# Optimization experiments

Hardware: AMD Instinct MI355X
Metric: run time of the kernel (lower is better)

Reference implementation:

```python
import jax, jax.numpy as jnp
import numpy as np

M1, N1, M2, N2, RANK = 64, 64, 64, 64, 256
TOKENS = 8192  # batch 4 * seq 2048, flattened


def setup_inputs() -> dict:
    key = jax.random.key(0)
    k_x, k_c1, k_c2, k_b = jax.random.split(key, 4)
    x = jax.random.normal(k_x, (TOKENS, N1 * N2), dtype=jnp.float32)
    # scale cores so reconstructed weight has reasonable magnitude
    core1 = jax.random.normal(k_c1, (M1, N1, RANK), dtype=jnp.float32) * 0.05
    core2 = jax.random.normal(k_c2, (RANK, M2, N2), dtype=jnp.float32) * 0.05
    bias = jax.random.normal(k_b, (M1 * M2,), dtype=jnp.float32)
    return {"x": x, "core1": core1, "core2": core2, "bias": bias}


def reference(x, core1, core2, bias):
    # contract_mpo: [m1,n1,r] x [r,m2,n2] -> [m1,n1,m2,n2]
    t = jnp.einsum('mnr,rpq->mnpq', core1, core2)
    # permute(0,2,1,3) then view -> weight [m1*m2, n1*n2] = [out, in]
    weight = t.transpose(0, 2, 1, 3).reshape(M1 * M2, N1 * N2)
    # nn.functional.linear: x @ W^T + b
    return x @ weight.T + bias
```

## Files before the change

### kernel.cpp

```cpp
#include <hip/hip_runtime.h>
#include <hip/hip_bf16.h>
#include <stdint.h>


#define TOKENS 8192
#define DIN    4096
#define DOUT   4096
#define RANK   256
#define GEMM_K 4096

typedef __attribute__((ext_vector_type(8))) short   short8;
typedef __attribute__((ext_vector_type(4))) float   floatx4;

__device__ __forceinline__ unsigned short f2bf(float f) {
  union { float f; unsigned u; } v; v.f = f;
  unsigned r = v.u + 0x7FFFu + ((v.u >> 16) & 1u);
  return (unsigned short)(r >> 16);
}

__device__ __forceinline__ void gl2lds16(const void* g, void* l) {
  __builtin_amdgcn_global_load_lds(
      (const __attribute__((address_space(1))) unsigned int*)g,
      (__attribute__((address_space(3))) unsigned int*)l,
      16, 0, 0);
}

__global__ __launch_bounds__(256) void k_f32_to_bf16(const float* __restrict__ src,
                                                     unsigned short* __restrict__ dst,
                                                     int n) {
  int i = (blockIdx.x * 256 + threadIdx.x) * 8;
  if (i >= n) return;
  float4 a = *(const float4*)(src + i);
  float4 b = *(const float4*)(src + i + 4);
  short8 o;
  o[0] = (short)f2bf(a.x); o[1] = (short)f2bf(a.y);
  o[2] = (short)f2bf(a.z); o[3] = (short)f2bf(a.w);
  o[4] = (short)f2bf(b.x); o[5] = (short)f2bf(b.y);
  o[6] = (short)f2bf(b.z); o[7] = (short)f2bf(b.w);
  *(short8*)(dst + i) = o;
}

__global__ __launch_bounds__(256) void k_transpose_c2(const float* __restrict__ c2,
                                                      unsigned short* __restrict__ c2t) {
  __shared__ float tile[64][65];
  const int p0 = blockIdx.x * 64;
  const int r0 = blockIdx.y * 64;
  {
    const int px = threadIdx.x & 63;
    const int rb = threadIdx.x >> 6;
    for (int s = 0; s < 16; ++s) {
      int r = rb + s * 4;
      tile[r][px] = c2[(size_t)(r0 + r) * 4096 + p0 + px];
    }
  }
  __syncthreads();
  {
    const int rx = threadIdx.x & 63;
    const int pb = threadIdx.x >> 6;
    for (int s = 0; s < 16; ++s) {
      int p = pb + s * 4;
      c2t[(size_t)(p0 + p) * 256 + r0 + rx] = f2bf(tile[rx][p]);
    }
  }
}

template <int K, int BK, bool PERM>
__global__ __launch_bounds__(256) void k_gemm_bt(const unsigned short* __restrict__ A,
                                                 const unsigned short* __restrict__ B,
                                                 float* __restrict__ outF,
                                                 unsigned short* __restrict__ outW,
                                                 const float* __restrict__ bias) {
  constexpr int ROWB   = BK * 2;
  constexpr int CM     = BK / 8 - 1;
  constexpr int ROUNDS = BK / 16;
  constexpr int KK     = BK / 32;

  __shared__ __align__(16) unsigned short As[128 * BK];
  __shared__ __align__(16) unsigned short Bs[128 * BK];

  const int tid  = threadIdx.x;
  const int lane = tid & 63;
  const int wave = tid >> 6;
  const int m0 = blockIdx.y * 128;
  const int n0 = blockIdx.x * 128;

  const int waveM = (wave & 1) * 64;
  const int waveN = (wave >> 1) * 64;
  const int l15  = lane & 15;
  const int quad = lane >> 4;

  floatx4 acc[4][4];
#pragma unroll
  for (int i = 0; i < 4; ++i)
#pragma unroll
    for (int j = 0; j < 4; ++j) acc[i][j] = (floatx4)0.0f;

  const size_t rowBytes = (size_t)K * 2;

  for (int kt = 0; kt < K; kt += BK) {
    __syncthreads();
#pragma unroll
    for (int j = 0; j < ROUNDS; ++j) {
      const int flat = (j * 4 + wave) * 1024 + lane * 16;
      const int row  = flat / ROWB;
      const int c    = (flat >> 4) & CM;
      const int cs   = c ^ (row & CM);
      const int ldsb = (j * 4 + wave) * 1024;
      gl2lds16((const char*)A + (size_t)(m0 + row) * rowBytes + (size_t)kt * 2 + cs * 16,
               (char*)As + ldsb);
      gl2lds16((const char*)B + (size_t)(n0 + row) * rowBytes + (size_t)kt * 2 + cs * 16,
               (char*)Bs + ldsb);
    }
    __syncthreads();

#pragma unroll
    for (int kk = 0; kk < KK; ++kk) {
      short8 af[4], bfr[4];
#pragma unroll
      for (int mi = 0; mi < 4; ++mi) {
        const int row = waveM + mi * 16 + l15;
        const int cs  = (kk * 4 + quad) ^ (row & CM);
        af[mi] = *(const short8*)(As + row * BK + cs * 8);
      }
#pragma unroll
      for (int ni = 0; ni < 4; ++ni) {
        const int row = waveN + ni * 16 + l15;
        const int cs  = (kk * 4 + quad) ^ (row & CM);
        bfr[ni] = *(const short8*)(Bs + row * BK + cs * 8);
      }
#pragma unroll
      for (int mi = 0; mi < 4; ++mi)
#pragma unroll
        for (int ni = 0; ni < 4; ++ni)
          acc[mi][ni] = __builtin_amdgcn_mfma_f32_16x16x32_bf16(af[mi], bfr[ni], acc[mi][ni], 0, 0, 0);
    }
  }

  if (!PERM) {
#pragma unroll
    for (int ni = 0; ni < 4; ++ni) {
      const int col = n0 + waveN + ni * 16 + l15;
      const float bv = bias[col];
#pragma unroll
      for (int mi = 0; mi < 4; ++mi) {
        const int rowb = m0 + waveM + mi * 16 + quad * 4;
#pragma unroll
        for (int r = 0; r < 4; ++r)
          outF[(size_t)(rowb + r) * DOUT + col] = acc[mi][ni][r] + bv;
      }
    }
  } else {
#pragma unroll
    for (int ni = 0; ni < 4; ++ni) {
      const int bcol = n0 + waveN + ni * 16 + l15;
      const int m2 = bcol >> 6, n2 = bcol & 63;
#pragma unroll
      for (int mi = 0; mi < 4; ++mi) {
        const int arow0 = m0 + waveM + mi * 16 + quad * 4;
#pragma unroll
        for (int r = 0; r < 4; ++r) {
          const int arow = arow0 + r;
          const int m1 = arow >> 6, n1 = arow & 63;
          outW[(size_t)(m1 * 64 + m2) * 4096 + (n1 * 64 + n2)] = f2bf(acc[mi][ni][r]);
        }
      }
    }
  }
}


__global__ __launch_bounds__(512, 2) void k_gemm256(const unsigned short* __restrict__ A,
                                                    const unsigned short* __restrict__ B,
                                                    float* __restrict__ out,
                                                    const float* __restrict__ bias) {
  __shared__ __align__(16) unsigned short As[2][2][8192];
  __shared__ __align__(16) unsigned short Bs[2][2][8192];

  const int tid  = threadIdx.x;
  const int lane = tid & 63;
  const int wave = tid >> 6;

  const int id  = blockIdx.y * gridDim.x + blockIdx.x;
  const int nid = (id & 7) * 64 + (id >> 3);
  const int bx  = nid & 15;
  const int by  = nid >> 4;
  const int m0  = by * 256;
  const int n0  = bx * 256;

  const int waveM = (wave >> 2) << 7;
  const int waveN = (wave & 3) << 6;
  const int l15   = lane & 15;
  const int quad  = lane >> 4;

  const int rsw = (quad ^ ((l15 >> 2) & 2)) * 8;
  const int srow   = wave * 16 + (lane >> 2);
  const int schunk = (lane & 3) ^ ((lane >> 4) & 2);

  floatx4 acc[8][4];
#pragma unroll
  for (int i = 0; i < 8; ++i)
#pragma unroll
    for (int j = 0; j < 4; ++j) acc[i][j] = (floatx4)0.0f;

#define STAGE(LDSHALF, GBASE, R0, KBYTE)                                          \
  {                                                                               \
    _Pragma("unroll")                                                             \
    for (int j_ = 0; j_ < 2; ++j_) {                                              \
      const char* src_ = (const char*)(GBASE) +                                   \
          (size_t)((R0) + j_ * 128 + srow) * (size_t)(GEMM_K * 2) +               \
          (size_t)(KBYTE) + schunk * 16;                                          \
      gl2lds16(src_, (char*)(LDSHALF) + j_ * 8192 + wave * 1024);                 \
    }                                                                             \
  }

#define PHASE(BUF, KH, MH, DO_STAGE, DO_VMCNT)                                    \
  {                                                                               \
    const unsigned short* pa_ = &As[BUF][KH][0];                                  \
    short8 af_[4];                                                                \
    if ((MH) == 0) {                                                              \
      const unsigned short* pb_ = &Bs[BUF][KH][0];                                \
      _Pragma("unroll")                                                           \
      for (int i_ = 0; i_ < 4; ++i_)                                              \
        bfv[i_] = *(const short8*)(pb_ + (waveN + i_ * 16 + l15) * 32 + rsw);     \
    }                                                                             \
    _Pragma("unroll")                                                             \
    for (int i_ = 0; i_ < 4; ++i_)                                                \
      af_[i_] = *(const short8*)(pa_ + (waveM + ((MH) * 4 + i_) * 16 + l15) * 32 + rsw); \
    DO_STAGE;                                                                     \
    if (DO_VMCNT) asm volatile("s_waitcnt vmcnt(4)" ::: "memory");                \
    asm volatile("s_barrier" ::: "memory");                                       \
    __builtin_amdgcn_sched_barrier(0);                                            \
    __builtin_amdgcn_s_setprio(1);                                                \
    _Pragma("unroll")                                                             \
    for (int i_ = 0; i_ < 4; ++i_)                                                \
      _Pragma("unroll")                                                           \
      for (int n_ = 0; n_ < 4; ++n_)                                              \
        acc[(MH) * 4 + i_][n_] = __builtin_amdgcn_mfma_f32_16x16x32_bf16(         \
            af_[i_], bfv[n_], acc[(MH) * 4 + i_][n_], 0, 0, 0);                   \
    __builtin_amdgcn_s_setprio(0);                                                \
    asm volatile("s_barrier" ::: "memory");                                       \
  }

#define KTILE(C, KTN)                                                             \
  {                                                                               \
    PHASE(C, 0, 0, STAGE(&As[1 - (C)][0][0], A, m0, (KTN) * 2), 0)                \
    PHASE(C, 0, 1, STAGE(&Bs[1 - (C)][0][0], B, n0, (KTN) * 2), 1)                \
    PHASE(C, 1, 0, STAGE(&As[1 - (C)][1][0], A, m0, (KTN) * 2 + 64), 0)           \
    PHASE(C, 1, 1, STAGE(&Bs[1 - (C)][1][0], B, n0, (KTN) * 2 + 64), 1)           \
  }

  STAGE(&As[0][0][0], A, m0, 0);
  STAGE(&Bs[0][0][0], B, n0, 0);
  STAGE(&As[0][1][0], A, m0, 64);
  STAGE(&Bs[0][1][0], B, n0, 64);
  asm volatile("s_waitcnt vmcnt(0)" ::: "memory");
  asm volatile("s_barrier" ::: "memory");

  short8 bfv[4];
  for (int kt = 0; kt < GEMM_K; kt += 128) {
    const int ktn0 = kt + 64;
    KTILE(0, ktn0)
    const int ktn1 = (kt + 128 < GEMM_K) ? (kt + 128) : 0;
    KTILE(1, ktn1)
  }

#undef KTILE
#undef PHASE
#undef STAGE

#pragma unroll
  for (int ni = 0; ni < 4; ++ni) {
    const int col = n0 + waveN + ni * 16 + l15;
    const float bv = bias[col];
#pragma unroll
    for (int mi = 0; mi < 8; ++mi) {
      const int row0 = m0 + waveM + mi * 16 + quad * 4;
#pragma unroll
      for (int r = 0; r < 4; ++r)
        out[(size_t)(row0 + r) * DOUT + col] = acc[mi][ni][r] + bv;
    }
  }
}

extern "C" void kernel_launch(void* const* d_in, const int* in_sizes, int n_in,
                              void* d_out, int out_size, void* d_ws, size_t ws_size,
                              hipStream_t stream) {
  const float* x    = (const float*)d_in[0];
  const float* c1   = (const float*)d_in[1];
  const float* c2   = (const float*)d_in[2];
  const float* bias = (const float*)d_in[3];
  float* out = (float*)d_out;

  char* ws = (char*)d_ws;
  unsigned short* xb  = (unsigned short*)ws;
  unsigned short* Wb  = (unsigned short*)(ws + 67108864);
  unsigned short* c1b = (unsigned short*)(ws + 67108864 + 33554432);
  unsigned short* c2t = (unsigned short*)(ws + 67108864 + 33554432 + 2097152);

  k_f32_to_bf16<<<(TOKENS * DIN) / 2048, 256, 0, stream>>>(x, xb, TOKENS * DIN);
  k_f32_to_bf16<<<(64 * 64 * RANK) / 2048, 256, 0, stream>>>(c1, c1b, 64 * 64 * RANK);
  k_transpose_c2<<<dim3(64, 4), 256, 0, stream>>>(c2, c2t);

  k_gemm_bt<RANK, 32, true><<<dim3(32, 32), 256, 0, stream>>>(c1b, c2t, nullptr, Wb, nullptr);
  k_gemm256<<<dim3(16, 32), 512, 0, stream>>>(xb, Wb, out, bias);
}
```

Before: 509.9 us.

## Software-pipeline LDS fragment reads with MFMA and cut barriers per k-tile

Restructures the GEMM main loop so the A/B fragments for the next MFMA group are read from LDS while the current group computes. Double-buffered register fragments (af0/af1, bfvA/bfvB) are added, and the number of barriers per k-tile drops from eight to two, with a vmcnt(2) wait. This targets LDS-read latency and barrier stalls. In exchange it uses more registers, which could pressure occupancy at 2 blocks of 512 threads per CU, and the sync placement must keep the reads of the next buffer correctly ordered.

```diff
diff --git a/kernel.cpp b/kernel.cpp
--- a/kernel.cpp
+++ b/kernel.cpp
@@ -168,7 +168,6 @@
   }
 }
 
-
 __global__ __launch_bounds__(512, 2) void k_gemm256(const unsigned short* __restrict__ A,
                                                     const unsigned short* __restrict__ B,
                                                     float* __restrict__ out,
@@ -201,6 +200,8 @@
   for (int i = 0; i < 8; ++i)
 #pragma unroll
     for (int j = 0; j < 4; ++j) acc[i][j] = (floatx4)0.0f;
+
+  short8 af0[4], af1[4], bfvA[4], bfvB[4];
 
 #define STAGE(LDSHALF, GBASE, R0, KBYTE)                                          \
   {                                                                               \
@@ -213,40 +214,57 @@
     }                                                                             \
   }
 
-#define PHASE(BUF, KH, MH, DO_STAGE, DO_VMCNT)                                    \
-  {                                                                               \
-    const unsigned short* pa_ = &As[BUF][KH][0];                                  \
-    short8 af_[4];                                                                \
-    if ((MH) == 0) {                                                              \
-      const unsigned short* pb_ = &Bs[BUF][KH][0];                                \
-      _Pragma("unroll")                                                           \
-      for (int i_ = 0; i_ < 4; ++i_)                                              \
-        bfv[i_] = *(const short8*)(pb_ + (waveN + i_ * 16 + l15) * 32 + rsw);     \
-    }                                                                             \
+#define READ_AF(DST, BUF, KH, MH)                                                 \
+  _Pragma("unroll")                                                               \
+  for (int i_ = 0; i_ < 4; ++i_)                                                  \
+    DST[i_] = *(const short8*)(&As[BUF][KH][0] +                                  \
+               (waveM + ((MH) * 4 + i_) * 16 + l15) * 32 + rsw);
+
+#define READ_BF(DST, BUF, KH)                                                     \
+  _Pragma("unroll")                                                               \
+  for (int n_ = 0; n_ < 4; ++n_)                                                  \
+    DST[n_] = *(const short8*)(&Bs[BUF][KH][0] +                                  \
+               (waveN + n_ * 16 + l15) * 32 + rsw);
+
+#define MFMA16(AF, BF, MH)                                                        \
+  __builtin_amdgcn_s_setprio(1);                                                  \
+  _Pragma("unroll")                                                               \
+  for (int i_ = 0; i_ < 4; ++i_)                                                  \
     _Pragma("unroll")                                                             \
-    for (int i_ = 0; i_ < 4; ++i_)                                                \
-      af_[i_] = *(const short8*)(pa_ + (waveM + ((MH) * 4 + i_) * 16 + l15) * 32 + rsw); \
-    DO_STAGE;                                                                     \
-    if (DO_VMCNT) asm volatile("s_waitcnt vmcnt(4)" ::: "memory");                \
-    asm volatile("s_barrier" ::: "memory");                                       \
+    for (int n_ = 0; n_ < 4; ++n_)                                                \
+      acc[(MH) * 4 + i_][n_] = __builtin_amdgcn_mfma_f32_16x16x32_bf16(           \
+          AF[i_], BF[n_], acc[(MH) * 4 + i_][n_], 0, 0, 0);                       \
+  __builtin_amdgcn_s_setprio(0);
+
+#define SYNC2()                                                                   \
+  asm volatile("s_waitcnt vmcnt(2)" ::: "memory");                                \
+  asm volatile("s_barrier" ::: "memory");
+
+#define KTILE(C, KTN)                                                             \
+  {                        \
+    READ_AF(af1, C, 0, 1)                                                         \
+    STAGE(&As[1 - (C)][0][0], A, m0, (KTN) * 2)                                   \
     __builtin_amdgcn_sched_barrier(0);                                            \
-    __builtin_amdgcn_s_setprio(1);                                                \
-    _Pragma("unroll")                                                             \
-    for (int i_ = 0; i_ < 4; ++i_)                                                \
-      _Pragma("unroll")                                                           \
-      for (int n_ = 0; n_ < 4; ++n_)                                              \
-        acc[(MH) * 4 + i_][n_] = __builtin_amdgcn_mfma_f32_16x16x32_bf16(         \
-            af_[i_], bfv[n_], acc[(MH) * 4 + i_][n_], 0, 0, 0);                   \
-    __builtin_amdgcn_s_setprio(0);                                                \
-    asm volatile("s_barrier" ::: "memory");                                       \
-  }
-
-#define KTILE(C, KTN)                                                             \
-  {                                                                               \
-    PHASE(C, 0, 0, STAGE(&As[1 - (C)][0][0], A, m0, (KTN) * 2), 0)                \
-    PHASE(C, 0, 1, STAGE(&Bs[1 - (C)][0][0], B, n0, (KTN) * 2), 1)                \
-    PHASE(C, 1, 0, STAGE(&As[1 - (C)][1][0], A, m0, (KTN) * 2 + 64), 0)           \
-    PHASE(C, 1, 1, STAGE(&Bs[1 - (C)][1][0], B, n0, (KTN) * 2 + 64), 1)           \
+    MFMA16(af0, bfvA, 0)                                                          \
+                \
+    SYNC2()                                                                       \
+    READ_AF(af0, C, 1, 0)                                                         \
+    READ_BF(bfvB, C, 1)                                                           \
+    STAGE(&Bs[1 - (C)][0][0], B, n0, (KTN) * 2)                                   \
+    __builtin_amdgcn_sched_barrier(0);                                            \
+    MFMA16(af1, bfvA, 1)                                                          \
+                           \
+    READ_AF(af1, C, 1, 1)                                                         \
+    STAGE(&As[1 - (C)][1][0], A, m0, (KTN) * 2 + 64)                              \
+    __builtin_amdgcn_sched_barrier(0);                                            \
+    MFMA16(af0, bfvB, 0)                                                          \
+    \
+    SYNC2()                                                                       \
+    READ_AF(af0, 1 - (C), 0, 0)                                                   \
+    READ_BF(bfvA, 1 - (C), 0)                                                     \
+    STAGE(&Bs[1 - (C)][1][0], B, n0, (KTN) * 2 + 64)                              \
+    __builtin_amdgcn_sched_barrier(0);                                            \
+    MFMA16(af1, bfvB, 1)                                                          \
   }
 
   STAGE(&As[0][0][0], A, m0, 0);
@@ -255,17 +273,20 @@
   STAGE(&Bs[0][1][0], B, n0, 64);
   asm volatile("s_waitcnt vmcnt(0)" ::: "memory");
   asm volatile("s_barrier" ::: "memory");
-
-  short8 bfv[4];
+  READ_AF(af0, 0, 0, 0)
+  READ_BF(bfvA, 0, 0)
+
   for (int kt = 0; kt < GEMM_K; kt += 128) {
-    const int ktn0 = kt + 64;
-    KTILE(0, ktn0)
+    KTILE(0, kt + 64)
     const int ktn1 = (kt + 128 < GEMM_K) ? (kt + 128) : 0;
     KTILE(1, ktn1)
   }
 
 #undef KTILE
-#undef PHASE
+#undef SYNC2
+#undef MFMA16
+#undef READ_BF
+#undef READ_AF
 #undef STAGE
 
 #pragma unroll
```

Measured after the change: 506.9 us. About the same (-0.6%).

## Restructure GEMM main loop with 64-wide K LDS tiles and 4-phase schedule

Applied to the files above, without the earlier changes.

Changes the GEMM LDS layout from two 32-wide K halves per buffer to a single 64-wide K row (128 bytes) with an XOR swizzle over 8 chunks. Fragment loads now use inline ds_read_b128. The main loop becomes four MFMA quadrants per tile, each with explicit lgkmcnt waits and barriers, interleaving global-to-LDS prefetch of the next tile. The aim is fewer LDS bank conflicts, more reuse of A/B fragments across quadrants, and better overlap of loads with MFMA. In exchange it adds more barriers and more live fragment registers.

```diff
diff --git a/kernel.cpp b/kernel.cpp
--- a/kernel.cpp
+++ b/kernel.cpp
@@ -23,6 +23,10 @@
       (const __attribute__((address_space(1))) unsigned int*)g,
       (__attribute__((address_space(3))) unsigned int*)l,
       16, 0, 0);
+}
+
+__device__ __forceinline__ unsigned ldsaddr(const void* p) {
+  return (unsigned)(size_t)(const __attribute__((address_space(3))) char*)p;
 }
 
 __global__ __launch_bounds__(256) void k_f32_to_bf16(const float* __restrict__ src,
@@ -168,13 +172,12 @@
   }
 }
 
-
 __global__ __launch_bounds__(512, 2) void k_gemm256(const unsigned short* __restrict__ A,
                                                     const unsigned short* __restrict__ B,
                                                     float* __restrict__ out,
                                                     const float* __restrict__ bias) {
-  __shared__ __align__(16) unsigned short As[2][2][8192];
-  __shared__ __align__(16) unsigned short Bs[2][2][8192];
+  __shared__ __align__(1024) unsigned short As[2][16384];
+  __shared__ __align__(1024) unsigned short Bs[2][16384];
 
   const int tid  = threadIdx.x;
   const int lane = tid & 63;
@@ -192,9 +195,9 @@
   const int l15   = lane & 15;
   const int quad  = lane >> 4;
 
-  const int rsw = (quad ^ ((l15 >> 2) & 2)) * 8;
-  const int srow   = wave * 16 + (lane >> 2);
-  const int schunk = (lane & 3) ^ ((lane >> 4) & 2);
+  const unsigned x0 = (unsigned)((quad ^ (l15 & 7)) * 16);
+  const int srow    = lane >> 3;
+  const int schunk16 = ((lane & 7) ^ (lane >> 3)) * 16;
 
   floatx4 acc[8][4];
 #pragma unroll
@@ -202,82 +205,133 @@
 #pragma unroll
     for (int j = 0; j < 4; ++j) acc[i][j] = (floatx4)0.0f;
 
-#define STAGE(LDSHALF, GBASE, R0, KBYTE)                                          \
+  short8 afA[4][2], afB[4][2], bf0[2][2], bf1[2][2];
+
+#define BARRIER() asm volatile("s_barrier" ::: "memory")
+#define SCHED0()  __builtin_amdgcn_sched_barrier(0)
+
+#define SA(BUF, KTN, H)                                                           \
   {                                                                               \
     _Pragma("unroll")                                                             \
     for (int j_ = 0; j_ < 2; ++j_) {                                              \
-      const char* src_ = (const char*)(GBASE) +                                   \
-          (size_t)((R0) + j_ * 128 + srow) * (size_t)(GEMM_K * 2) +               \
-          (size_t)(KBYTE) + schunk * 16;                                          \
-      gl2lds16(src_, (char*)(LDSHALF) + j_ * 8192 + wave * 1024);                 \
+      const char* src_ = (const char*)A +                                         \
+          (size_t)(m0 + (H) * 128 + wave * 16 + j_ * 8 + srow) * 8192 +           \
+          (size_t)(KTN) * 2 + schunk16;                                           \
+      gl2lds16(src_, (char*)&As[BUF][0] + (H) * 16384 + wave * 2048 + j_ * 1024); \
     }                                                                             \
   }
 
-#define PHASE(BUF, KH, MH, DO_STAGE, DO_VMCNT)                                    \
+#define SB(BUF, KTN, H)                                                           \
   {                                                                               \
-    const unsigned short* pa_ = &As[BUF][KH][0];                                  \
-    short8 af_[4];                                                                \
-    if ((MH) == 0) {                                                              \
-      const unsigned short* pb_ = &Bs[BUF][KH][0];                                \
+    _Pragma("unroll")                                                             \
+    for (int j_ = 0; j_ < 2; ++j_) {                                              \
+      const char* src_ = (const char*)B +                                         \
+          (size_t)(n0 + (H) * 128 + wave * 16 + j_ * 8 + srow) * 8192 +           \
+          (size_t)(KTN) * 2 + schunk16;                                           \
+      gl2lds16(src_, (char*)&Bs[BUF][0] + (H) * 16384 + wave * 2048 + j_ * 1024); \
+    }                                                                             \
+  }
+
+#define R_AF(DST, BUF, MH)                                                        \
+  _Pragma("unroll")                                                               \
+  for (int mi_ = 0; mi_ < 4; ++mi_)                                               \
+    _Pragma("unroll")                                                             \
+    for (int kk_ = 0; kk_ < 2; ++kk_)                                             \
+      asm volatile("ds_read_b128 %0, %1" : "=v"(DST[mi_][kk_])                    \
+          : "v"(ldsaddr(&As[BUF][0]) +                                            \
+                (unsigned)((waveM + (MH) * 64 + mi_ * 16 + l15) * 128) +          \
+                (x0 ^ (unsigned)(kk_ * 64))));
+
+#define R_BF(DST, BUF, NH)                                                        \
+  _Pragma("unroll")                                                               \
+  for (int ni_ = 0; ni_ < 2; ++ni_)                                               \
+    _Pragma("unroll")                                                             \
+    for (int kk_ = 0; kk_ < 2; ++kk_)                                             \
+      asm volatile("ds_read_b128 %0, %1" : "=v"(DST[ni_][kk_])                    \
+          : "v"(ldsaddr(&Bs[BUF][0]) +                                            \
+                (unsigned)((waveN + (NH) * 32 + ni_ * 16 + l15) * 128) +          \
+                (x0 ^ (unsigned)(kk_ * 64))));
+
+#define LGKM0() { asm volatile("s_waitcnt lgkmcnt(0)"); SCHED0(); }
+#define LGKM8() { asm volatile("s_waitcnt lgkmcnt(8)"); }
+
+#define MM(MH, NH, AF, BF)                                                        \
+  __builtin_amdgcn_s_setprio(1);                                                  \
+  _Pragma("unroll")                                                               \
+  for (int kk_ = 0; kk_ < 2; ++kk_)                                               \
+    _Pragma("unroll")                                                             \
+    for (int mi_ = 0; mi_ < 4; ++mi_)                                             \
       _Pragma("unroll")                                                           \
-      for (int i_ = 0; i_ < 4; ++i_)                                              \
-        bfv[i_] = *(const short8*)(pb_ + (waveN + i_ * 16 + l15) * 32 + rsw);     \
-    }                                                                             \
-    _Pragma("unroll")                                                             \
-    for (int i_ = 0; i_ < 4; ++i_)                                                \
-      af_[i_] = *(const short8*)(pa_ + (waveM + ((MH) * 4 + i_) * 16 + l15) * 32 + rsw); \
-    DO_STAGE;                                                                     \
-    if (DO_VMCNT) asm volatile("s_waitcnt vmcnt(4)" ::: "memory");                \
-    asm volatile("s_barrier" ::: "memory");                                       \
-    __builtin_amdgcn_sched_barrier(0);                                            \
-    __builtin_amdgcn_s_setprio(1);                                                \
-    _Pragma("unroll")                                                             \
-    for (int i_ = 0; i_ < 4; ++i_)                                                \
-      _Pragma("unroll")                                                           \
-      for (int n_ = 0; n_ < 4; ++n_)                                              \
-        acc[(MH) * 4 + i_][n_] = __builtin_amdgcn_mfma_f32_16x16x32_bf16(         \
-            af_[i_], bfv[n_], acc[(MH) * 4 + i_][n_], 0, 0, 0);                   \
-    __builtin_amdgcn_s_setprio(0);                                                \
-    asm volatile("s_barrier" ::: "memory");                                       \
-  }
-
-#define KTILE(C, KTN)                                                             \
-  {                                                                               \
-    PHASE(C, 0, 0, STAGE(&As[1 - (C)][0][0], A, m0, (KTN) * 2), 0)                \
-    PHASE(C, 0, 1, STAGE(&Bs[1 - (C)][0][0], B, n0, (KTN) * 2), 1)                \
-    PHASE(C, 1, 0, STAGE(&As[1 - (C)][1][0], A, m0, (KTN) * 2 + 64), 0)           \
-    PHASE(C, 1, 1, STAGE(&Bs[1 - (C)][1][0], B, n0, (KTN) * 2 + 64), 1)           \
-  }
-
-  STAGE(&As[0][0][0], A, m0, 0);
-  STAGE(&Bs[0][0][0], B, n0, 0);
-  STAGE(&As[0][1][0], A, m0, 64);
-  STAGE(&Bs[0][1][0], B, n0, 64);
+      for (int ni_ = 0; ni_ < 2; ++ni_)                                           \
+        acc[(MH) * 4 + mi_][(NH) * 2 + ni_] =                                     \
+            __builtin_amdgcn_mfma_f32_16x16x32_bf16(                              \
+                AF[mi_][kk_], BF[ni_][kk_], acc[(MH) * 4 + mi_][(NH) * 2 + ni_],  \
+                0, 0, 0);                                                         \
+  __builtin_amdgcn_s_setprio(0);                                                  \
+  SCHED0();
+
+#define ITER(C, KTN)                                                              \
+  {                                                                       \
+    R_AF(afA, C, 0)                                                               \
+    R_BF(bf0, C, 0)                                                               \
+    SA(1 - (C), KTN, 0)                                                           \
+    SA(1 - (C), KTN, 1)                                                           \
+    LGKM8()                                                                       \
+    BARRIER();                                                                    \
+    LGKM0()                                                                       \
+    MM(0, 0, afA, bf0)                                                            \
+    BARRIER();                                                                    \
+                                                                          \
+    R_AF(afB, C, 1)                                                               \
+    SB(1 - (C), KTN, 0)                                                           \
+    SB(1 - (C), KTN, 1)                                                           \
+    BARRIER();                                                                    \
+    LGKM0()                                                                       \
+    MM(1, 0, afB, bf0)                                                            \
+    BARRIER();                                                                    \
+                                                                          \
+    R_BF(bf1, C, 1)                                                               \
+    BARRIER();                                                                    \
+    LGKM0()                                                                       \
+    MM(0, 1, afA, bf1)                                                            \
+    BARRIER();                                                                    \
+                                                                          \
+    asm volatile("s_waitcnt vmcnt(0)" ::: "memory");                              \
+    BARRIER();                                                                    \
+    MM(1, 1, afB, bf1)                                                            \
+    BARRIER();                                                                    \
+  }
+
+  SA(0, 0, 0) SA(0, 0, 1) SB(0, 0, 0) SB(0, 0, 1)
   asm volatile("s_waitcnt vmcnt(0)" ::: "memory");
-  asm volatile("s_barrier" ::: "memory");
-
-  short8 bfv[4];
+  BARRIER();
+
   for (int kt = 0; kt < GEMM_K; kt += 128) {
-    const int ktn0 = kt + 64;
-    KTILE(0, ktn0)
-    const int ktn1 = (kt + 128 < GEMM_K) ? (kt + 128) : 0;
-    KTILE(1, ktn1)
-  }
-
-#undef KTILE
-#undef PHASE
-#undef STAGE
-
-#pragma unroll
-  for (int ni = 0; ni < 4; ++ni) {
-    const int col = n0 + waveN + ni * 16 + l15;
+    ITER(0, kt + 64)
+    ITER(1, (kt + 128) & (GEMM_K - 1))
+  }
+
+#undef ITER
+#undef MM
+#undef LGKM8
+#undef LGKM0
+#undef R_BF
+#undef R_AF
+#undef SB
+#undef SA
+#undef SCHED0
+#undef BARRIER
+
+#pragma unroll
+  for (int b = 0; b < 4; ++b) {
+    const int col = n0 + waveN + (b >> 1) * 32 + (b & 1) * 16 + l15;
     const float bv = bias[col];
 #pragma unroll
-    for (int mi = 0; mi < 8; ++mi) {
-      const int row0 = m0 + waveM + mi * 16 + quad * 4;
+    for (int a = 0; a < 8; ++a) {
+      const int row0 = m0 + waveM + (a >> 2) * 64 + (a & 3) * 16 + quad * 4;
 #pragma unroll
       for (int r = 0; r < 4; ++r)
-        out[(size_t)(row0 + r) * DOUT + col] = acc[mi][ni][r] + bv;
+        out[(size_t)(row0 + r) * DOUT + col] = acc[a][b][r] + bv;
     }
   }
 }
```

Measured after the change: 1.023 ms. +100.6%, slower.
